# Kernel tuning notes

Hardware: AMD Instinct MI355X
Metric: run time of the kernel (lower is better)

Reference implementation:

```python
import jax, jax.numpy as jnp
import numpy as np

N_NODES = 100000
D_FEAT = 128
N_GATHER = 2000000
N_SEGMENTS = 250000


def setup_inputs() -> dict:
    key = jax.random.key(0)
    k1, k2, k3 = jax.random.split(key, 3)
    node_feature = jax.random.normal(k1, (N_NODES, D_FEAT), dtype=jnp.float32)
    batch_node_ids = jax.random.randint(k2, (N_GATHER,), 0, N_NODES, dtype=jnp.int64)
    batch_macro_node_ids = jax.random.randint(k3, (N_GATHER,), 0, N_SEGMENTS, dtype=jnp.int64)
    return {
        "node_feature": node_feature,
        "batch_node_ids": batch_node_ids,
        "batch_macro_node_ids": batch_macro_node_ids,
    }


def reference(node_feature, batch_node_ids, batch_macro_node_ids):
    # gather node features for every subgraph membership: [E, d]
    gathered = node_feature[batch_node_ids]
    # scatter-mean by macro (fragment) id, matching torch_scatter reduce='mean'
    seg_sum = jax.ops.segment_sum(gathered, batch_macro_node_ids, num_segments=N_SEGMENTS)
    counts = jax.ops.segment_sum(
        jnp.ones((batch_macro_node_ids.shape[0],), dtype=node_feature.dtype),
        batch_macro_node_ids,
        num_segments=N_SEGMENTS,
    )
    # empty segments -> 0 (torch_scatter clamps divisor to >=1)
    return seg_sum / jnp.maximum(counts, 1.0)[:, None]
```

## Files before the change

kernel.cpp:

```cpp
#include <hip/hip_runtime.h>
#include <hip/hip_fp16.h>


constexpr int N_NODES = 100000;
constexpr int D_FEAT  = 128;
constexpr int N_SEG   = 250000;

constexpr int BSHIFT     = 8;
constexpr int SEGS_PER_B = 1 << BSHIFT;
constexpr int NB         = (N_SEG + SEGS_PER_B - 1) >> BSHIFT;
constexpr int NB_PAD     = 1024;
constexpr int EPB        = 4096;
constexpr int CTH        = 512;
constexpr int CAP_B      = 4096;
constexpr int NID_BITS   = 17;
constexpr int NID_MASK   = (1 << NID_BITS) - 1;
constexpr int OVF_CAP    = 262144;

#define NP_CUR(ws)    ((int*)((char*)(ws) + 0))
#define NP_OVFC(ws)   ((int*)((char*)(ws) + 4096))
#define NP_PAIRS(ws)  ((int*)((char*)(ws) + (1u<<20)))
#define NP_OVF(ws)    ((int2*)((char*)(ws) + (18u<<20)))
#define NP_F16(ws)    ((char*)(ws) + (20u<<20))
constexpr size_t FP16_BYTES = (size_t)N_NODES * D_FEAT * 2;
constexpr size_t WS_NEED_H  = (size_t)(20u << 20) + FP16_BYTES;

#define RP_CNT(ws)     ((int*)((char*)(ws) + 0))
#define RP_OFF(ws)     ((int*)((char*)(ws) + (1u<<20)))
#define RP_BSUM(ws)    ((int*)((char*)(ws) + (2u<<20)))
#define RP_RANK(ws)    ((int*)((char*)(ws) + (4u<<20)))
#define RP_SORTED(ws)  ((int*)((char*)(ws) + (12u<<20)))
constexpr int SCAN_CHUNK  = 1024;
constexpr int SCAN_BLOCKS = (N_SEG + SCAN_CHUNK - 1) / SCAN_CHUNK;

typedef float nt4 __attribute__((ext_vector_type(4)));
typedef unsigned int ntu4 __attribute__((ext_vector_type(4)));


__global__ __launch_bounds__(CTH) void sp_bucket_scatter(
    const int* __restrict__ sid, const int* __restrict__ nid,
    int* __restrict__ cursor_g, int* __restrict__ pairs,
    int* __restrict__ ovf_cnt, int2* __restrict__ ovf, int n)
{
    __shared__ int hist[NB_PAD];
    __shared__ int dstb[NB_PAD];
    __shared__ int lpair[EPB];
    __shared__ unsigned short lbuck[EPB];
    __shared__ int sh[CTH];
    int tid = threadIdx.x;
    int e0  = blockIdx.x * EPB;
    int m   = min(EPB, n - e0);

    for (int i = tid; i < NB_PAD; i += CTH) hist[i] = 0;
    __syncthreads();
    for (int i = tid; i < m; i += CTH)
        atomicAdd(&hist[sid[e0 + i] >> BSHIFT], 1);
    __syncthreads();

    int b0 = 2 * tid, b1 = 2 * tid + 1;
    int h0 = hist[b0], h1 = hist[b1];
    sh[tid] = h0 + h1;
    __syncthreads();
    for (int o = 1; o < CTH; o <<= 1) {
        int t = (tid >= o) ? sh[tid - o] : 0;
        __syncthreads();
        sh[tid] += t;
        __syncthreads();
    }
    int excl = (tid > 0) ? sh[tid - 1] : 0;
    __syncthreads();
    hist[b0] = excl;
    hist[b1] = excl + h0;
    int a0 = (b0 < NB && h0 > 0) ? atomicAdd(&cursor_g[b0], h0) : 0;
    int a1 = (b1 < NB && h1 > 0) ? atomicAdd(&cursor_g[b1], h1) : 0;
    dstb[b0] = a0 - excl;
    dstb[b1] = a1 - (excl + h0);
    __syncthreads();

    for (int i = tid; i < m; i += CTH) {
        int s = sid[e0 + i], v = nid[e0 + i];
        int b = s >> BSHIFT;
        int r = atomicAdd(&hist[b], 1);
        lpair[r] = ((s & (SEGS_PER_B - 1)) << NID_BITS) | v;
        lbuck[r] = (unsigned short)b;
    }
    __syncthreads();

    for (int i = tid; i < m; i += CTH) {
        int b  = lbuck[i];
        int p  = dstb[b] + i;
        int pk = lpair[i];
        if (p < CAP_B) {
            pairs[b * CAP_B + p] = pk;
        } else {
            int o = atomicAdd(ovf_cnt, 1);
            if (o < OVF_CAP)
                ovf[o] = make_int2((b << BSHIFT) | (pk >> NID_BITS),
                                   pk & NID_MASK);
        }
    }
}


__global__ __launch_bounds__(256) void sp_cvt(
    const float* __restrict__ in, unsigned int* __restrict__ out, int n8,
    int* __restrict__ cursor_g, int* __restrict__ ovf_cnt)
{
    if (blockIdx.x == 0) {
        for (int k = threadIdx.x; k < NB; k += 256) cursor_g[k] = 0;
        if (threadIdx.x == 0) *ovf_cnt = 0;
    }
    int i = blockIdx.x * blockDim.x + threadIdx.x;
    if (i >= n8) return;
    const nt4* in4 = (const nt4*)in;
    nt4 v0 = __builtin_nontemporal_load(&in4[2 * i + 0]);
    nt4 v1 = __builtin_nontemporal_load(&in4[2 * i + 1]);
    __half2 h0 = __floats2half2_rn(v0.x, v0.y);
    __half2 h1 = __floats2half2_rn(v0.z, v0.w);
    __half2 h2 = __floats2half2_rn(v1.x, v1.y);
    __half2 h3 = __floats2half2_rn(v1.z, v1.w);
    ntu4 o;
    o.x = *(const unsigned int*)&h0;
    o.y = *(const unsigned int*)&h1;
    o.z = *(const unsigned int*)&h2;
    o.w = *(const unsigned int*)&h3;
    __builtin_nontemporal_store(o, (ntu4*)out + i);
}

__device__ __forceinline__ float2 h2f(unsigned short lo, unsigned short hi)
{
    __half2 h = __halves2half2(__ushort_as_half(lo), __ushort_as_half(hi));
    return __half22float2(h);
}

__device__ __forceinline__ void acc_h(float4& acc, const ushort4& b)
{
    float2 f01 = h2f(b.x, b.y);
    float2 f23 = h2f(b.z, b.w);
    acc.x += f01.x; acc.y += f01.y; acc.z += f23.x; acc.w += f23.y;
}


__global__ __launch_bounds__(CTH) void sp_reduce_f(
    const ushort4* __restrict__ feat16,
    const int* __restrict__ pairs,
    const int* __restrict__ cursor_g,
    const int* __restrict__ ovf_cnt,
    const int2* __restrict__ ovf,
    float4* __restrict__ out4)
{
    __shared__ int cnt[SEGS_PER_B];
    __shared__ int beg[SEGS_PER_B];
    __shared__ int cur[SEGS_PER_B];
    __shared__ int sh[SEGS_PER_B];
    __shared__ int lp[CAP_B];
    __shared__ int snid[CAP_B];
    int B = blockIdx.x, tid = threadIdx.x;
    int total = cursor_g[B];
    int mc = min(total, CAP_B);
    const int* bp = pairs + (size_t)B * CAP_B;

    if (tid < SEGS_PER_B) cnt[tid] = 0;
    __syncthreads();
    for (int i = tid; i < mc; i += CTH) {
        int p = bp[i];
        lp[i] = p;
        atomicAdd(&cnt[(p >> NID_BITS) & (SEGS_PER_B - 1)], 1);
    }
    __syncthreads();

    int c = (tid < SEGS_PER_B) ? cnt[tid] : 0;
    if (tid < SEGS_PER_B) sh[tid] = c;
    __syncthreads();
    for (int o = 1; o < SEGS_PER_B; o <<= 1) {
        int t = (tid < SEGS_PER_B && tid >= o) ? sh[tid - o] : 0;
        __syncthreads();
        if (tid < SEGS_PER_B) sh[tid] += t;
        __syncthreads();
    }
    if (tid < SEGS_PER_B) { beg[tid] = sh[tid] - c; cur[tid] = sh[tid] - c; }
    __syncthreads();

    for (int i = tid; i < mc; i += CTH) {
        int p  = lp[i];
        int sl = (p >> NID_BITS) & (SEGS_PER_B - 1);
        int r  = atomicAdd(&cur[sl], 1);
        snid[r] = p & NID_MASK;
    }
    __syncthreads();

    int ovfB = total - mc;
    int ovn  = (ovfB > 0) ? min(*ovf_cnt, OVF_CAP) : 0;

    int hw = tid >> 5, lane = tid & 31;
    for (int t = 0; t < SEGS_PER_B / 16; ++t) {
        int sl = hw * (SEGS_PER_B / 16) + t;
        int s  = (B << BSHIFT) + sl;
        if (s >= N_SEG) continue;
        int nst = cnt[sl], bg = beg[sl];
        int m2  = (nst < 32) ? nst : 32;
        int myid = (lane < m2) ? snid[bg + lane] : 0;

        float4 acc0 = make_float4(0.f, 0.f, 0.f, 0.f);
        float4 acc1 = make_float4(0.f, 0.f, 0.f, 0.f);
        if (m2 > 0) {
            int last = m2 - 1;
            for (int j0 = 0; j0 < m2; j0 += 8) {
                int id[8];
#pragma unroll
                for (int k = 0; k < 8; ++k) {
                    int jj = j0 + k;
                    id[k] = __shfl(myid, (jj < last) ? jj : last, 32);
                }
                ushort4 b[8];
#pragma unroll
                for (int k = 0; k < 8; ++k)
                    b[k] = feat16[(size_t)id[k] * 32 + lane];
#pragma unroll
                for (int k = 0; k < 8; ++k) {
                    if (j0 + k < m2) {
                        if (k & 1) acc_h(acc1, b[k]);
                        else       acc_h(acc0, b[k]);
                    }
                }
            }
            for (int k = 32; k < nst; ++k)
                acc_h(acc0, feat16[(size_t)snid[bg + k] * 32 + lane]);
        }
        int ntrue = nst;
        if (ovfB > 0) {
            for (int k = 0; k < ovn; ++k) {
                int2 e = ovf[k];
                if (e.x == s) {
                    acc_h(acc0, feat16[(size_t)e.y * 32 + lane]);
                    ++ntrue;
                }
            }
        }
        float inv = 1.0f / (float)((ntrue > 0) ? ntrue : 1);
        nt4 r;
        r.x = (acc0.x + acc1.x) * inv;
        r.y = (acc0.y + acc1.y) * inv;
        r.z = (acc0.z + acc1.z) * inv;
        r.w = (acc0.w + acc1.w) * inv;
        __builtin_nontemporal_store(
            r, reinterpret_cast<nt4*>(out4) + (size_t)s * 32 + lane);
    }
}


__global__ __launch_bounds__(256) void sp_hist_rank(
    const int* __restrict__ sid, int* __restrict__ cnt,
    int* __restrict__ rank, int n)
{
    int i = blockIdx.x * blockDim.x + threadIdx.x;
    if (i >= n) return;
    int s = sid[i];
    rank[i] = atomicAdd(&cnt[s], 1);
}

__global__ __launch_bounds__(256) void sp_scan_local(
    const int* __restrict__ cnt, int* __restrict__ off, int* __restrict__ bsum)
{
    __shared__ int sh[256];
    int tid  = threadIdx.x;
    int base = blockIdx.x * SCAN_CHUNK + tid * 4;
    int v0 = (base + 0 < N_SEG) ? cnt[base + 0] : 0;
    int v1 = (base + 1 < N_SEG) ? cnt[base + 1] : 0;
    int v2 = (base + 2 < N_SEG) ? cnt[base + 2] : 0;
    int v3 = (base + 3 < N_SEG) ? cnt[base + 3] : 0;
    sh[tid] = v0 + v1 + v2 + v3;
    __syncthreads();
    for (int o = 1; o < 256; o <<= 1) {
        int t = (tid >= o) ? sh[tid - o] : 0;
        __syncthreads();
        sh[tid] += t;
        __syncthreads();
    }
    int excl = (tid > 0) ? sh[tid - 1] : 0;
    if (base + 0 < N_SEG) off[base + 0] = excl;
    if (base + 1 < N_SEG) off[base + 1] = excl + v0;
    if (base + 2 < N_SEG) off[base + 2] = excl + v0 + v1;
    if (base + 3 < N_SEG) off[base + 3] = excl + v0 + v1 + v2;
    if (tid == 255) bsum[blockIdx.x] = sh[255];
}

__global__ __launch_bounds__(256) void sp_scan_blocks(int* __restrict__ bsum)
{
    __shared__ int sh[256];
    int tid = threadIdx.x;
    int v = (tid < SCAN_BLOCKS) ? bsum[tid] : 0;
    sh[tid] = v;
    __syncthreads();
    for (int o = 1; o < 256; o <<= 1) {
        int t = (tid >= o) ? sh[tid - o] : 0;
        __syncthreads();
        sh[tid] += t;
        __syncthreads();
    }
    if (tid < SCAN_BLOCKS) bsum[tid] = sh[tid] - v;
}

__global__ __launch_bounds__(256) void sp_reorder_rank(
    const int* __restrict__ nid, const int* __restrict__ sid,
    const int* __restrict__ off, const int* __restrict__ bsum,
    const int* __restrict__ rank, int* __restrict__ sorted_nid, int n)
{
    int i = blockIdx.x * blockDim.x + threadIdx.x;
    if (i >= n) return;
    int s = sid[i];
    sorted_nid[off[s] + bsum[s >> 10] + rank[i]] = nid[i];
}

__global__ __launch_bounds__(256) void sp_reduce(
    const float4* __restrict__ feat4,
    const int* __restrict__ sorted_nid,
    const int* __restrict__ off,
    const int* __restrict__ bsum,
    const int* __restrict__ cnt,
    float4* __restrict__ out4)
{
    int seg  = blockIdx.x * 8 + (threadIdx.x >> 5);
    int lane = threadIdx.x & 31;
    if (seg >= N_SEG) return;

    int n   = cnt[seg];
    int beg = off[seg] + bsum[seg >> 10];
    int m   = (n < 32) ? n : 32;
    int myid = (lane < m) ? sorted_nid[beg + lane] : 0;

    float4 acc0 = make_float4(0.f, 0.f, 0.f, 0.f);
    float4 acc1 = make_float4(0.f, 0.f, 0.f, 0.f);

    if (m > 0) {
        int last = m - 1;
        for (int j0 = 0; j0 < m; j0 += 8) {
            int id[8];
#pragma unroll
            for (int k = 0; k < 8; ++k) {
                int jj = j0 + k;
                id[k] = __shfl(myid, (jj < last) ? jj : last, 32);
            }
            float4 b[8];
#pragma unroll
            for (int k = 0; k < 8; ++k)
                b[k] = feat4[(size_t)id[k] * 32 + lane];
#pragma unroll
            for (int k = 0; k < 8; ++k) {
                if (j0 + k < m) {
                    if (k & 1) {
                        acc1.x += b[k].x; acc1.y += b[k].y;
                        acc1.z += b[k].z; acc1.w += b[k].w;
                    } else {
                        acc0.x += b[k].x; acc0.y += b[k].y;
                        acc0.z += b[k].z; acc0.w += b[k].w;
                    }
                }
            }
        }
        for (int k = 32; k < n; ++k) {
            int nk = sorted_nid[beg + k];
            float4 a = feat4[(size_t)nk * 32 + lane];
            acc0.x += a.x; acc0.y += a.y; acc0.z += a.z; acc0.w += a.w;
        }
    }

    float inv = 1.0f / (float)((n > 0) ? n : 1);
    nt4 r;
    r.x = (acc0.x + acc1.x) * inv;
    r.y = (acc0.y + acc1.y) * inv;
    r.z = (acc0.z + acc1.z) * inv;
    r.w = (acc0.w + acc1.w) * inv;
    __builtin_nontemporal_store(
        r, reinterpret_cast<nt4*>(out4) + (size_t)seg * 32 + lane);
}


extern "C" void kernel_launch(void* const* d_in, const int* in_sizes, int n_in,
                              void* d_out, int out_size, void* d_ws, size_t ws_size,
                              hipStream_t stream) {
    const float* feat = (const float*)d_in[0];
    const int*   nid  = (const int*)d_in[1];
    const int*   sid  = (const int*)d_in[2];
    const int n_edges = in_sizes[1];

    if (ws_size >= WS_NEED_H && n_edges > 0) {
        int* cursor  = NP_CUR(d_ws);
        int* ovfc    = NP_OVFC(d_ws);
        int2* ovf    = NP_OVF(d_ws);
        int* pairs   = NP_PAIRS(d_ws);
        unsigned int* feat16 = (unsigned int*)NP_F16(d_ws);

        int n8 = N_NODES * D_FEAT / 8;
        sp_cvt<<<(n8 + 255) / 256, 256, 0, stream>>>(feat, feat16, n8,
                                                     cursor, ovfc);
        int sb = (n_edges + EPB - 1) / EPB;
        sp_bucket_scatter<<<sb, CTH, 0, stream>>>(sid, nid, cursor, pairs,
                                                  ovfc, ovf, n_edges);
        sp_reduce_f<<<NB, CTH, 0, stream>>>((const ushort4*)feat16, pairs,
                                            cursor, ovfc, ovf,
                                            (float4*)d_out);
    } else {
        int* cnt    = RP_CNT(d_ws);
        int* off    = RP_OFF(d_ws);
        int* bsum   = RP_BSUM(d_ws);
        int* rank   = RP_RANK(d_ws);
        int* sorted = RP_SORTED(d_ws);
        int eb = (n_edges + 255) / 256;
        int rb = (N_SEG + 7) / 8;

        hipMemsetAsync(d_ws, 0, (size_t)(1u << 20), stream);
        sp_hist_rank<<<eb, 256, 0, stream>>>(sid, cnt, rank, n_edges);
        sp_scan_local<<<SCAN_BLOCKS, 256, 0, stream>>>(cnt, off, bsum);
        sp_scan_blocks<<<1, 256, 0, stream>>>(bsum);
        sp_reorder_rank<<<eb, 256, 0, stream>>>(nid, sid, off, bsum, rank,
                                                sorted, n_edges);
        sp_reduce<<<rb, 256, 0, stream>>>((const float4*)feat, sorted, off,
                                          bsum, cnt, (float4*)d_out);
    }
}
```

Baseline: 294.5 us.

## Fuse fp16 conversion into bucket scatter kernel and pad global cursors

Merges the fp32-to-fp16 feature conversion into the bucket-scatter launch as extra blocks, so conversion and scatter run concurrently in one grid. Cursor reset moves to a memset. Global bucket cursors are spaced 64 bytes apart to cut atomic contention on shared cache lines. Edges per scatter block double to 8192, which halves the number of global cursor atomics but doubles per-block LDS use and lowers occupancy.

```diff
diff --git a/kernel.cpp b/kernel.cpp
--- a/kernel.cpp
+++ b/kernel.cpp
@@ -10,15 +10,16 @@
 constexpr int SEGS_PER_B = 1 << BSHIFT;
 constexpr int NB         = (N_SEG + SEGS_PER_B - 1) >> BSHIFT;
 constexpr int NB_PAD     = 1024;
-constexpr int EPB        = 4096;
+constexpr int EPB        = 8192;
 constexpr int CTH        = 512;
 constexpr int CAP_B      = 4096;
 constexpr int NID_BITS   = 17;
 constexpr int NID_MASK   = (1 << NID_BITS) - 1;
 constexpr int OVF_CAP    = 262144;
+constexpr int CUR_STRIDE = 16;
 
 #define NP_CUR(ws)    ((int*)((char*)(ws) + 0))
-#define NP_OVFC(ws)   ((int*)((char*)(ws) + 4096))
+#define NP_OVFC(ws)   ((int*)((char*)(ws) + 64512))
 #define NP_PAIRS(ws)  ((int*)((char*)(ws) + (1u<<20)))
 #define NP_OVF(ws)    ((int2*)((char*)(ws) + (18u<<20)))
 #define NP_F16(ws)    ((char*)(ws) + (20u<<20))
@@ -37,10 +38,12 @@
 typedef unsigned int ntu4 __attribute__((ext_vector_type(4)));
 
 
-__global__ __launch_bounds__(CTH) void sp_bucket_scatter(
+__global__ __launch_bounds__(CTH) void sp_fused_cvt_scatter(
+    const float* __restrict__ feat, unsigned int* __restrict__ feat16,
+    int n8,
     const int* __restrict__ sid, const int* __restrict__ nid,
     int* __restrict__ cursor_g, int* __restrict__ pairs,
-    int* __restrict__ ovf_cnt, int2* __restrict__ ovf, int n)
+    int* __restrict__ ovf_cnt, int2* __restrict__ ovf, int n, int sb)
 {
     __shared__ int hist[NB_PAD];
     __shared__ int dstb[NB_PAD];
@@ -48,8 +51,29 @@
     __shared__ unsigned short lbuck[EPB];
     __shared__ int sh[CTH];
     int tid = threadIdx.x;
-    int e0  = blockIdx.x * EPB;
-    int m   = min(EPB, n - e0);
+
+    if ((int)blockIdx.x >= sb) {
+        int i = (blockIdx.x - sb) * CTH + tid;
+        if (i < n8) {
+            const nt4* in4 = (const nt4*)feat;
+            nt4 v0 = __builtin_nontemporal_load(&in4[2 * i + 0]);
+            nt4 v1 = __builtin_nontemporal_load(&in4[2 * i + 1]);
+            __half2 h0 = __floats2half2_rn(v0.x, v0.y);
+            __half2 h1 = __floats2half2_rn(v0.z, v0.w);
+            __half2 h2 = __floats2half2_rn(v1.x, v1.y);
+            __half2 h3 = __floats2half2_rn(v1.z, v1.w);
+            ntu4 o;
+            o.x = *(const unsigned int*)&h0;
+            o.y = *(const unsigned int*)&h1;
+            o.z = *(const unsigned int*)&h2;
+            o.w = *(const unsigned int*)&h3;
+            __builtin_nontemporal_store(o, (ntu4*)feat16 + i);
+        }
+        return;
+    }
+
+    int e0 = blockIdx.x * EPB;
+    int m  = min(EPB, n - e0);
 
     for (int i = tid; i < NB_PAD; i += CTH) hist[i] = 0;
     __syncthreads();
@@ -71,8 +95,8 @@
     __syncthreads();
     hist[b0] = excl;
     hist[b1] = excl + h0;
-    int a0 = (b0 < NB && h0 > 0) ? atomicAdd(&cursor_g[b0], h0) : 0;
-    int a1 = (b1 < NB && h1 > 0) ? atomicAdd(&cursor_g[b1], h1) : 0;
+    int a0 = (b0 < NB && h0 > 0) ? atomicAdd(&cursor_g[b0 * CUR_STRIDE], h0) : 0;
+    int a1 = (b1 < NB && h1 > 0) ? atomicAdd(&cursor_g[b1 * CUR_STRIDE], h1) : 0;
     dstb[b0] = a0 - excl;
     dstb[b1] = a1 - (excl + h0);
     __syncthreads();
@@ -102,31 +126,6 @@
 }
 
 
-__global__ __launch_bounds__(256) void sp_cvt(
-    const float* __restrict__ in, unsigned int* __restrict__ out, int n8,
-    int* __restrict__ cursor_g, int* __restrict__ ovf_cnt)
-{
-    if (blockIdx.x == 0) {
-        for (int k = threadIdx.x; k < NB; k += 256) cursor_g[k] = 0;
-        if (threadIdx.x == 0) *ovf_cnt = 0;
-    }
-    int i = blockIdx.x * blockDim.x + threadIdx.x;
-    if (i >= n8) return;
-    const nt4* in4 = (const nt4*)in;
-    nt4 v0 = __builtin_nontemporal_load(&in4[2 * i + 0]);
-    nt4 v1 = __builtin_nontemporal_load(&in4[2 * i + 1]);
-    __half2 h0 = __floats2half2_rn(v0.x, v0.y);
-    __half2 h1 = __floats2half2_rn(v0.z, v0.w);
-    __half2 h2 = __floats2half2_rn(v1.x, v1.y);
-    __half2 h3 = __floats2half2_rn(v1.z, v1.w);
-    ntu4 o;
-    o.x = *(const unsigned int*)&h0;
-    o.y = *(const unsigned int*)&h1;
-    o.z = *(const unsigned int*)&h2;
-    o.w = *(const unsigned int*)&h3;
-    __builtin_nontemporal_store(o, (ntu4*)out + i);
-}
-
 __device__ __forceinline__ float2 h2f(unsigned short lo, unsigned short hi)
 {
     __half2 h = __halves2half2(__ushort_as_half(lo), __ushort_as_half(hi));
@@ -156,7 +155,7 @@
     __shared__ int lp[CAP_B];
     __shared__ int snid[CAP_B];
     int B = blockIdx.x, tid = threadIdx.x;
-    int total = cursor_g[B];
+    int total = cursor_g[B * CUR_STRIDE];
     int mc = min(total, CAP_B);
     const int* bp = pairs + (size_t)B * CAP_B;
 
@@ -391,12 +390,13 @@
         int* pairs   = NP_PAIRS(d_ws);
         unsigned int* feat16 = (unsigned int*)NP_F16(d_ws);
 
+        hipMemsetAsync(d_ws, 0, 65536, stream);
         int n8 = N_NODES * D_FEAT / 8;
-        sp_cvt<<<(n8 + 255) / 256, 256, 0, stream>>>(feat, feat16, n8,
-                                                     cursor, ovfc);
-        int sb = (n_edges + EPB - 1) / EPB;
-        sp_bucket_scatter<<<sb, CTH, 0, stream>>>(sid, nid, cursor, pairs,
-                                                  ovfc, ovf, n_edges);
+        int sb  = (n_edges + EPB - 1) / EPB;
+        int cvb = (n8 + CTH - 1) / CTH;
+        sp_fused_cvt_scatter<<<sb + cvb, CTH, 0, stream>>>(
+            feat, feat16, n8, sid, nid, cursor, pairs, ovfc, ovf,
+            n_edges, sb);
         sp_reduce_f<<<NB, CTH, 0, stream>>>((const ushort4*)feat16, pairs,
                                             cursor, ovfc, ovf,
                                             (float4*)d_out);
```

Measured after the change: 279.9 us. -5.0%, faster.
